# Performance work log

Hardware: AMD Instinct MI355X
Metric: run time of the kernel (lower is better)

The kernel has to match this reference:

```python
import jax, jax.numpy as jnp
import numpy as np

B, N, DIM = 4, 4096, 768
H = 12
DH = DIM // H          # 64
S = 16                 # num_segments
M = N // S             # 256 segment_len
SCALE = DH ** -0.5


def setup_inputs() -> dict:
    key = jax.random.key(0)
    ks = jax.random.split(key, 7)
    std = DIM ** -0.5
    return {
        "x": jax.random.normal(ks[0], (B, N, DIM), dtype=jnp.float32),
        "Wq": jax.random.normal(ks[1], (DIM, DIM), dtype=jnp.float32) * std,
        "Wkv": jax.random.normal(ks[2], (DIM, DIM), dtype=jnp.float32) * std,
        "Wo": jax.random.normal(ks[3], (DIM, DIM), dtype=jnp.float32) * std,
        "bo": jax.random.normal(ks[4], (DIM,), dtype=jnp.float32) * 0.02,
        "Wo0": jax.random.normal(ks[5], (DIM, DIM), dtype=jnp.float32) * std,
        "bo0": jax.random.normal(ks[6], (DIM,), dtype=jnp.float32) * 0.02,
    }


def _rotary_freqs(n, dh, dtype):
    # lucidrains RotaryEmbedding: inv_freq over even dims, emb = cat(freqs, freqs)
    inv_freq = 1.0 / (10000.0 ** (jnp.arange(0, dh, 2, dtype=jnp.float32) / dh))
    t = jnp.arange(n, dtype=jnp.float32)
    freqs = jnp.einsum("n,f->nf", t, inv_freq)           # (n, dh/2)
    return jnp.concatenate([freqs, freqs], axis=-1).astype(dtype)  # (n, dh)


def _rotate_half(t):
    # '... (j d) -> ... j d', j=2 ; (-x2, x1)
    x1, x2 = jnp.split(t, 2, axis=-1)
    return jnp.concatenate([-x2, x1], axis=-1)


def _apply_rotary(freqs, t):
    # freqs: (1, n, dh) broadcast over (bh, n, dh); rot_dim == dh here
    return t * jnp.cos(freqs) + _rotate_half(t) * jnp.sin(freqs)


def reference(x, Wq, Wkv, Wo, bo, Wo0, bo0):
    b, n, dim = x.shape
    q = x @ Wq            # (b, n, dim), bias-free
    kv = x @ Wkv          # shared K==V projection

    def to_heads(t):      # 'b n (h d) -> (b h) n d'
        return t.reshape(b, n, H, DH).transpose(0, 2, 1, 3).reshape(b * H, n, DH)

    q, kv = to_heads(q), to_heads(kv)

    freqs = _rotary_freqs(n, DH, x.dtype)[None, :, :]    # (1, n, dh)
    q = _apply_rotary(freqs, q)
    kv = _apply_rotary(freqs, kv)

    q = q * SCALE
    c = b * H
    qs = q.reshape(c, S, M, DH)
    kvs = kv.reshape(c, S, M, DH)

    # adjacent-segment KV windows: segment t attends to [t-1, t] for t>=1
    kvs_ccs = jnp.concatenate([kvs[:, :-1], kvs[:, 1:]], axis=2)  # (c, S-1, 2M, dh)
    qs_ccs = qs[:, 1:]                                            # (c, S-1, M, dh)

    lsim = jnp.einsum("csmd,csnd->csmn", qs_ccs, kvs_ccs)         # (c, S-1, M, 2M)
    attn1 = jax.nn.softmax(lsim, axis=-1)
    out1 = jnp.einsum("csmn,csnd->csmd", attn1, kvs_ccs)          # (c, S-1, M, dh)

    # global (self) attention within first segment
    q0, kv0 = qs[:, 0], kvs[:, 0]                                 # (c, M, dh)
    sim0 = jnp.einsum("cmd,cnd->cmn", q0, kv0)
    attn0 = jax.nn.softmax(sim0, axis=-1)
    out0 = jnp.einsum("cmn,cnd->cmd", attn0, kv0)                 # (c, M, dh)

    def merge_heads(t, nn):  # '(b h) nn d -> b nn (h d)'
        return t.reshape(b, H, nn, DH).transpose(0, 2, 1, 3).reshape(b, nn, H * DH)

    out_1 = merge_heads(out1.reshape(c, (S - 1) * M, DH), (S - 1) * M)
    out_0 = merge_heads(out0, M)

    out_1o = out_1 @ Wo + bo
    out_0o = out_0 @ Wo0 + bo0
    return jnp.concatenate([out_0o, out_1o], axis=1)              # (b, n, dim)
```

## Files before the change

### kernel.cpp

```cpp
#include <hip/hip_runtime.h>
#include <hip/hip_bf16.h>


typedef float f32x4 __attribute__((ext_vector_type(4)));
typedef short bf16x8 __attribute__((ext_vector_type(8)));

#define DEV static __device__ __forceinline__

DEV short f2bf(float f) {
  union { __hip_bfloat16 h; unsigned short u; } cv;
  cv.h = __float2bfloat16(f);
  return (short)cv.u;
}

DEV f32x4 fz4() { f32x4 z = {0.f, 0.f, 0.f, 0.f}; return z; }

DEV void gload16(const void* g, void* l) {
  __builtin_amdgcn_global_load_lds((const __attribute__((address_space(1))) void*)g,
                                   (__attribute__((address_space(3))) void*)l, 16, 0, 0);
}

__global__ void __launch_bounds__(256) k_rope(float* __restrict__ cosT,
                                              float* __restrict__ sinT) {
  int idx = blockIdx.x * 256 + threadIdx.x;
  int pos = idx >> 5, jm = idx & 31;
  float invf = exp2f(-(float)jm * (13.287712379549449f / 32.0f));
  float th = (float)pos * invf;
  cosT[idx] = cosf(th);
  sinT[idx] = sinf(th);
}

__global__ void __launch_bounds__(256) k_cvtx(const float* __restrict__ x,
                                              short* __restrict__ xb) {
  int i = (blockIdx.x * 256 + threadIdx.x) * 8;
  float4 a = *(const float4*)(x + i);
  float4 b = *(const float4*)(x + i + 4);
  bf16x8 v;
  v[0] = f2bf(a.x); v[1] = f2bf(a.y); v[2] = f2bf(a.z); v[3] = f2bf(a.w);
  v[4] = f2bf(b.x); v[5] = f2bf(b.y); v[6] = f2bf(b.z); v[7] = f2bf(b.w);
  *(bf16x8*)(xb + i) = v;
}

__global__ void __launch_bounds__(256) k_transw(const float* __restrict__ Wq,
                                                const float* __restrict__ Wkv,
                                                const float* __restrict__ Wo,
                                                const float* __restrict__ Wo0,
                                                short* __restrict__ WtQKV,
                                                short* __restrict__ WtO) {
  __shared__ float t[64][65];
  int z = blockIdx.z;
  const float* src = (z == 0) ? Wq : (z == 1) ? Wkv : (z == 2) ? Wo : Wo0;
  short* dst = (z < 2) ? (WtQKV + (size_t)z * (768 * 768))
                       : (WtO + (size_t)(z - 2) * (768 * 768));
  int k0 = blockIdx.x * 64, j0 = blockIdx.y * 64;
  int tc = threadIdx.x & 63, tr = threadIdx.x >> 6;
#pragma unroll
  for (int i = 0; i < 16; i++) {
    int r = i * 4 + tr;
    t[tc][r] = src[(size_t)(k0 + r) * 768 + j0 + tc];
  }
  __syncthreads();
#pragma unroll
  for (int i = 0; i < 16; i++) {
    int r = i * 4 + tr;
    dst[(size_t)(j0 + r) * 768 + k0 + tc] = f2bf(t[r][tc]);
  }
}

#define QSTAGE64(Abuf, Bbuf, Abase, Bbase, kt)                                 \
  {                                                                            \
    int cci = (((tid & 7) ^ ((tid >> 3) & 7)) << 4);                           \
    _Pragma("unroll") for (int i = 0; i < 4; i++) {                            \
      int rowi = i * 32 + (tid >> 3);                                          \
      gload16((Abase) + (size_t)(r0 + rowi) * 1536 + (kt) * 128 + cci,         \
              (char*)(Abuf) + i * 4096 + wid * 1024);                          \
      gload16((Bbase) + (size_t)(j0 + rowi) * 1536 + (kt) * 128 + cci,         \
              (char*)(Bbuf) + i * 4096 + wid * 1024);                          \
    }                                                                          \
  }

__global__ void __launch_bounds__(256, 2) k_gemm_qkv(
    const short* __restrict__ xb, const short* __restrict__ Wt,
    const float* __restrict__ cosT, const float* __restrict__ sinT,
    short* __restrict__ Qb, short* __restrict__ KVb) {
  __shared__ short Al[2][8192];
  __shared__ short Bl[2][8192];
  int bid = blockIdx.x;
  int xcd = bid & 7, loc = bid >> 3;
  int r0 = (xcd * 16 + loc / 12) * 128;
  int cbk = loc % 12;
  bool isQ = cbk < 6;
  int cbl = isQ ? cbk : cbk - 6;
  const char* Ab = (const char*)xb;
  const char* Bb = (const char*)(Wt + (isQ ? (size_t)0 : (size_t)(768 * 768)));
  int j0 = cbl * 128;
  int tid = threadIdx.x, lane = tid & 63, wid = tid >> 6;
  int wr = wid >> 1, wc = wid & 1;
  int l15 = lane & 15, lg = lane >> 4;
  int swz = (l15 & 7) << 4;

  f32x4 acc[4][4];
#pragma unroll
  for (int i = 0; i < 4; i++)
#pragma unroll
    for (int j = 0; j < 4; j++) acc[i][j] = fz4();

  QSTAGE64(Al[0], Bl[0], Ab, Bb, 0)
  for (int kt = 0; kt < 12; kt++) {
    int cb = kt & 1;
    __syncthreads();
    if (kt + 1 < 12) QSTAGE64(Al[cb ^ 1], Bl[cb ^ 1], Ab, Bb, kt + 1)
    const char* Ac = (const char*)Al[cb];
    const char* Bc = (const char*)Bl[cb];
#pragma unroll
    for (int kk = 0; kk < 2; kk++) {
      bf16x8 af[4], bfr[4];
#pragma unroll
      for (int mr = 0; mr < 4; mr++)
        af[mr] = *(const bf16x8*)(Ac + (wr * 64 + mr * 16 + l15) * 128 +
                                  ((kk * 64 + lg * 16) ^ swz));
#pragma unroll
      for (int nc = 0; nc < 4; nc++)
        bfr[nc] = *(const bf16x8*)(Bc + (wc * 64 + nc * 16 + l15) * 128 +
                                   ((kk * 64 + lg * 16) ^ swz));
#pragma unroll
      for (int mr = 0; mr < 4; mr++)
#pragma unroll
        for (int nc = 0; nc < 4; nc++)
          acc[mr][nc] = __builtin_amdgcn_mfma_f32_16x16x32_bf16(af[mr], bfr[nc], acc[mr][nc], 0, 0, 0);
    }
  }

  int h = 2 * cbl + wc;
  short* Ob = isQ ? Qb : KVb;
  float scl = isQ ? 0.18033688011112042f : 1.0f;
#pragma unroll
  for (int mr = 0; mr < 4; mr++) {
#pragma unroll
    for (int rg = 0; rg < 4; rg++) {
      int r = r0 + wr * 64 + mr * 16 + lg * 4 + rg;
      int b = r >> 12, pos = r & 4095;
      const float* cT = cosT + pos * 32;
      const float* sT = sinT + pos * 32;
      float c0 = cT[l15], s0 = sT[l15];
      float c1 = cT[16 + l15], s1 = sT[16 + l15];
      float v0 = acc[mr][0][rg], v1 = acc[mr][1][rg];
      float v2 = acc[mr][2][rg], v3 = acc[mr][3][rg];
      size_t base = ((size_t)((b * 12 + h) * 4096 + pos)) * 64 + l15;
      Ob[base]      = f2bf((v0 * c0 - v2 * s0) * scl);
      Ob[base + 16] = f2bf((v1 * c1 - v3 * s1) * scl);
      Ob[base + 32] = f2bf((v2 * c0 + v0 * s0) * scl);
      Ob[base + 48] = f2bf((v3 * c1 + v1 * s1) * scl);
    }
  }
}

__global__ void __launch_bounds__(256) k_transkv(const short* __restrict__ KVb,
                                                 short* __restrict__ KVt) {
  __shared__ short T[64][72];
  int c = blockIdx.x;
  int pt = blockIdx.y;
  int t = threadIdx.x;
  int ch = t & 7, rr = t >> 3;
#pragma unroll
  for (int i = 0; i < 2; i++) {
    int p = rr + i * 32;
    bf16x8 v = *(const bf16x8*)&KVb[((size_t)c * 4096 + pt * 64 + p) * 64 + ch * 8];
    *(bf16x8*)&T[p][ch * 8] = v;
  }
  __syncthreads();
#pragma unroll
  for (int i = 0; i < 2; i++) {
    int d = rr + i * 32;
    bf16x8 v;
#pragma unroll
    for (int j = 0; j < 8; j++) {
      int cc = ch * 8 + j;
      int g = cc >> 5, sig = cc & 31;
      int p = g * 32 + 4 * (sig >> 3) + (sig & 3) + 16 * ((sig >> 2) & 1);
      v[j] = T[p][d];
    }
    *(bf16x8*)&KVt[((size_t)c * 64 + d) * 4096 + pt * 64 + ch * 8] = v;
  }
}

#define STAGE(buf, kk0)                                                        \
  {                                                                            \
    _Pragma("unroll") for (int i = 0; i < 2; i++) {                            \
      gload16(KVc + (size_t)((kk0) + i * 32 + krow) * 128 + ksrccol,           \
              (char*)Kl[buf] + i * 4096 + wid * 1024);                         \
      gload16(KVtc + ((size_t)(i * 32 + krow) * 4096 + (kk0)) * 2 + ksrccol,   \
              (char*)Vl[buf] + i * 4096 + wid * 1024);                         \
    }                                                                          \
  }

__global__ void __launch_bounds__(256, 4) k_attn(const short* __restrict__ Qb,
                                                 const short* __restrict__ KVbp,
                                                 const short* __restrict__ KVtp,
                                                 short* __restrict__ AO) {
  __shared__ short Kl[2][4096];
  __shared__ short Vl[2][4096];
  int bid = blockIdx.x;
  int orig = (bid & 7) * 192 + (bid >> 3);
  int c = orig >> 5;
  int e = orig & 31;
  int s = (e < 2) ? 0 : ((e - 2) >> 1) + 1;
  int qh = (e < 2) ? e : (e - 2) & 1;
  int NC = (s == 0) ? 4 : 8;
  int Kbase = (s == 0) ? 0 : (s - 1) * 256;

  int tid = threadIdx.x, lane = tid & 63, wid = tid >> 6;
  int l15 = lane & 15, lg = lane >> 4;
  const char* KVc = (const char*)(KVbp + (size_t)c * 4096 * 64);
  const char* KVtc = (const char*)(KVtp + (size_t)c * 64 * 4096);

  int krow = tid >> 3;
  int ksrccol = ((tid & 7) * 16) ^ ((krow & 7) << 4);
  int swz = (l15 & 7) << 4;

  int q0 = s * 256 + qh * 128 + wid * 32;
  bf16x8 qf[2][2];
#pragma unroll
  for (int qt = 0; qt < 2; qt++) {
    const short* Qr = Qb + ((size_t)c * 4096 + q0 + qt * 16 + l15) * 64 + lg * 8;
    qf[qt][0] = *(const bf16x8*)Qr;
    qf[qt][1] = *(const bf16x8*)(Qr + 32);
  }

  const f32x4 mi = {-32.f, -32.f, -32.f, -32.f};
  bf16x8 ones;
#pragma unroll
  for (int j = 0; j < 8; j++) ones[j] = (short)0x3F80;

  f32x4 oacc[2][4];
  f32x4 lacc[2];
#pragma unroll
  for (int qt = 0; qt < 2; qt++) {
    lacc[qt] = fz4();
#pragma unroll
    for (int vt = 0; vt < 4; vt++) oacc[qt][vt] = fz4();
  }

  STAGE(0, Kbase)
  for (int ch = 0; ch < NC; ch++) {
    int cb = ch & 1;
    __syncthreads();
    if (ch + 1 < NC) STAGE(cb ^ 1, Kbase + (ch + 1) * 64)
    const char* Kb_ = (const char*)Kl[cb];
    const char* Vb_ = (const char*)Vl[cb];
#pragma unroll
    for (int u = 0; u < 2; u++) {
      f32x4 z[2][2];
#pragma unroll
      for (int t2 = 0; t2 < 2; t2++) {
        const char* Kp = Kb_ + ((2 * u + t2) * 16 + l15) * 128;
        bf16x8 kf0 = *(const bf16x8*)(Kp + ((lg * 16) ^ swz));
        bf16x8 kf1 = *(const bf16x8*)(Kp + ((64 + lg * 16) ^ swz));
        __builtin_amdgcn_s_setprio(1);
#pragma unroll
        for (int qt = 0; qt < 2; qt++) {
          f32x4 zz = __builtin_amdgcn_mfma_f32_16x16x32_bf16(kf0, qf[qt][0], mi, 0, 0, 0);
          zz = __builtin_amdgcn_mfma_f32_16x16x32_bf16(kf1, qf[qt][1], zz, 0, 0, 0);
          z[qt][t2] = zz;
        }
        __builtin_amdgcn_s_setprio(0);
      }
      bf16x8 pf[2];
#pragma unroll
      for (int qt = 0; qt < 2; qt++) {
#pragma unroll
        for (int t2 = 0; t2 < 2; t2++)
#pragma unroll
          for (int r = 0; r < 4; r++)
            pf[qt][t2 * 4 + r] = f2bf(exp2f(z[qt][t2][r]));
      }
      bf16x8 vf[4];
#pragma unroll
      for (int vt = 0; vt < 4; vt++)
        vf[vt] = *(const bf16x8*)(Vb_ + (vt * 16 + l15) * 128 +
                                  ((u * 64 + lg * 16) ^ swz));
      __builtin_amdgcn_s_setprio(1);
#pragma unroll
      for (int qt = 0; qt < 2; qt++) {
#pragma unroll
        for (int vt = 0; vt < 4; vt++)
          oacc[qt][vt] = __builtin_amdgcn_mfma_f32_16x16x32_bf16(pf[qt], vf[vt], oacc[qt][vt], 0, 0, 0);
        lacc[qt] = __builtin_amdgcn_mfma_f32_16x16x32_bf16(pf[qt], ones, lacc[qt], 0, 0, 0);
      }
      __builtin_amdgcn_s_setprio(0);
    }
  }

  int bq = c / 12, hh = c % 12;
#pragma unroll
  for (int qt = 0; qt < 2; qt++) {
    float rinv[4];
#pragma unroll
    for (int r = 0; r < 4; r++) rinv[r] = 1.0f / lacc[qt][r];
#pragma unroll
    for (int vt = 0; vt < 4; vt++)
#pragma unroll
      for (int r = 0; r < 4; r++) {
        size_t row = (size_t)bq * 4096 + q0 + qt * 16 + lg * 4 + r;
        AO[row * 768 + hh * 64 + vt * 16 + l15] = f2bf(oacc[qt][vt][r] * rinv[r]);
      }
  }
}

__global__ void __launch_bounds__(256, 2) k_gemm_out(
    const short* __restrict__ AO, const short* __restrict__ Wt,
    const float* __restrict__ bo, const float* __restrict__ bo0,
    float* __restrict__ out) {
  __shared__ short Al[2][8192];
  __shared__ short Bl[2][8192];
  int bid = blockIdx.x;
  int xcd = bid & 7, loc = bid >> 3;
  int r0 = (xcd * 16 + loc / 6) * 128;
  int j0 = (loc % 6) * 128;
  bool o0sel = (r0 & 4095) < 256;
  const char* Ab = (const char*)AO;
  const char* Bb = (const char*)(Wt + (o0sel ? (size_t)1 : (size_t)0) * (768 * 768));
  const float* bias = o0sel ? bo0 : bo;
  int tid = threadIdx.x, lane = tid & 63, wid = tid >> 6;
  int wr = wid >> 1, wc = wid & 1;
  int l15 = lane & 15, lg = lane >> 4;
  int swz = (l15 & 7) << 4;

  f32x4 acc[4][4];
#pragma unroll
  for (int i = 0; i < 4; i++)
#pragma unroll
    for (int j = 0; j < 4; j++) acc[i][j] = fz4();

  QSTAGE64(Al[0], Bl[0], Ab, Bb, 0)
  for (int kt = 0; kt < 12; kt++) {
    int cb = kt & 1;
    __syncthreads();
    if (kt + 1 < 12) QSTAGE64(Al[cb ^ 1], Bl[cb ^ 1], Ab, Bb, kt + 1)
    const char* Ac = (const char*)Al[cb];
    const char* Bc = (const char*)Bl[cb];
#pragma unroll
    for (int kk = 0; kk < 2; kk++) {
      bf16x8 af[4], bfr[4];
#pragma unroll
      for (int mr = 0; mr < 4; mr++)
        af[mr] = *(const bf16x8*)(Ac + (wr * 64 + mr * 16 + l15) * 128 +
                                  ((kk * 64 + lg * 16) ^ swz));
#pragma unroll
      for (int nc = 0; nc < 4; nc++)
        bfr[nc] = *(const bf16x8*)(Bc + (wc * 64 + nc * 16 + l15) * 128 +
                                   ((kk * 64 + lg * 16) ^ swz));
#pragma unroll
      for (int mr = 0; mr < 4; mr++)
#pragma unroll
        for (int nc = 0; nc < 4; nc++)
          acc[mr][nc] = __builtin_amdgcn_mfma_f32_16x16x32_bf16(af[mr], bfr[nc], acc[mr][nc], 0, 0, 0);
    }
  }

  float bs[4];
#pragma unroll
  for (int nc = 0; nc < 4; nc++) bs[nc] = bias[j0 + wc * 64 + nc * 16 + l15];
#pragma unroll
  for (int mr = 0; mr < 4; mr++)
#pragma unroll
    for (int rg = 0; rg < 4; rg++) {
      size_t r = (size_t)r0 + wr * 64 + mr * 16 + lg * 4 + rg;
      float* op = out + r * 768 + j0 + wc * 64 + l15;
      op[0]  = acc[mr][0][rg] + bs[0];
      op[16] = acc[mr][1][rg] + bs[1];
      op[32] = acc[mr][2][rg] + bs[2];
      op[48] = acc[mr][3][rg] + bs[3];
    }
}

extern "C" void kernel_launch(void* const* d_in, const int* in_sizes, int n_in,
                              void* d_out, int out_size, void* d_ws, size_t ws_size,
                              hipStream_t stream) {
  (void)in_sizes; (void)n_in; (void)out_size; (void)ws_size;
  const float* x   = (const float*)d_in[0];
  const float* Wq  = (const float*)d_in[1];
  const float* Wkv = (const float*)d_in[2];
  const float* Wo  = (const float*)d_in[3];
  const float* bo  = (const float*)d_in[4];
  const float* Wo0 = (const float*)d_in[5];
  const float* bo0 = (const float*)d_in[6];
  float* out = (float*)d_out;

  char* ws = (char*)d_ws;
  short* xb    = (short*)(ws + 0);
  short* AO    = xb;
  short* Qb    = (short*)(ws + 25165824);
  short* KVb   = (short*)(ws + 50331648);
  short* KVt   = (short*)(ws + 75497472);
  short* WtQKV = (short*)(ws + 75497472);
  float* cosT  = (float*)(ws + 77856768);
  float* sinT  = (float*)(ws + 78381056);
  short* WtO   = (short*)(ws + 100663296);

  k_rope<<<512, 256, 0, stream>>>(cosT, sinT);
  k_cvtx<<<6144, 256, 0, stream>>>(x, xb);
  k_transw<<<dim3(12, 12, 4), 256, 0, stream>>>(Wq, Wkv, Wo, Wo0, WtQKV, WtO);
  k_gemm_qkv<<<1536, 256, 0, stream>>>(xb, WtQKV, cosT, sinT, Qb, KVb);
  k_transkv<<<dim3(48, 64), 256, 0, stream>>>(KVb, KVt);
  k_attn<<<1536, 256, 0, stream>>>(Qb, KVb, KVt, AO);
  k_gemm_out<<<768, 256, 0, stream>>>(AO, WtO, bo, bo0, out);
}
```

Baseline: 160.0 us.

## Fuse KV transpose into QKV GEMM epilogue and interleave rope cos/sin tables

The QKV GEMM epilogue now also writes the transposed KV layout itself, staging tiles through shared memory with a permuted, swizzled order, so the separate k_transkv kernel launch and its extra read of KVb are dropped. The rope cos and sin tables are merged into one float2 array so each epilogue lookup is a single load. Workspace offsets are rearranged and the fused path is used only when the workspace is large enough. Otherwise it falls back to the old separate transpose. The cost is an extra LDS round trip and two barriers in the KV blocks' epilogue.

```diff
diff --git a/kernel.cpp b/kernel.cpp
--- a/kernel.cpp
+++ b/kernel.cpp
@@ -20,14 +20,12 @@
                                    (__attribute__((address_space(3))) void*)l, 16, 0, 0);
 }
 
-__global__ void __launch_bounds__(256) k_rope(float* __restrict__ cosT,
-                                              float* __restrict__ sinT) {
+__global__ void __launch_bounds__(256) k_rope(float2* __restrict__ csT) {
   int idx = blockIdx.x * 256 + threadIdx.x;
   int pos = idx >> 5, jm = idx & 31;
   float invf = exp2f(-(float)jm * (13.287712379549449f / 32.0f));
   float th = (float)pos * invf;
-  cosT[idx] = cosf(th);
-  sinT[idx] = sinf(th);
+  csT[idx] = make_float2(cosf(th), sinf(th));
 }
 
 __global__ void __launch_bounds__(256) k_cvtx(const float* __restrict__ x,
@@ -81,10 +79,10 @@
 
 __global__ void __launch_bounds__(256, 2) k_gemm_qkv(
     const short* __restrict__ xb, const short* __restrict__ Wt,
-    const float* __restrict__ cosT, const float* __restrict__ sinT,
-    short* __restrict__ Qb, short* __restrict__ KVb) {
-  __shared__ short Al[2][8192];
-  __shared__ short Bl[2][8192];
+    const float2* __restrict__ csT,
+    short* __restrict__ Qb, short* __restrict__ KVb,
+    short* __restrict__ KVtw) {
+  __shared__ short Lsh[4][8192];
   int bid = blockIdx.x;
   int xcd = bid & 7, loc = bid >> 3;
   int r0 = (xcd * 16 + loc / 12) * 128;
@@ -105,13 +103,13 @@
 #pragma unroll
     for (int j = 0; j < 4; j++) acc[i][j] = fz4();
 
-  QSTAGE64(Al[0], Bl[0], Ab, Bb, 0)
+  QSTAGE64(Lsh[0], Lsh[2], Ab, Bb, 0)
   for (int kt = 0; kt < 12; kt++) {
     int cb = kt & 1;
     __syncthreads();
-    if (kt + 1 < 12) QSTAGE64(Al[cb ^ 1], Bl[cb ^ 1], Ab, Bb, kt + 1)
-    const char* Ac = (const char*)Al[cb];
-    const char* Bc = (const char*)Bl[cb];
+    if (kt + 1 < 12) QSTAGE64(Lsh[cb ^ 1], Lsh[2 + (cb ^ 1)], Ab, Bb, kt + 1)
+    const char* Ac = (const char*)Lsh[cb];
+    const char* Bc = (const char*)Lsh[2 + cb];
 #pragma unroll
     for (int kk = 0; kk < 2; kk++) {
       bf16x8 af[4], bfr[4];
@@ -134,23 +132,56 @@
   int h = 2 * cbl + wc;
   short* Ob = isQ ? Qb : KVb;
   float scl = isQ ? 0.18033688011112042f : 1.0f;
+  short ovv[4][4][4];
 #pragma unroll
   for (int mr = 0; mr < 4; mr++) {
 #pragma unroll
     for (int rg = 0; rg < 4; rg++) {
       int r = r0 + wr * 64 + mr * 16 + lg * 4 + rg;
       int b = r >> 12, pos = r & 4095;
-      const float* cT = cosT + pos * 32;
-      const float* sT = sinT + pos * 32;
-      float c0 = cT[l15], s0 = sT[l15];
-      float c1 = cT[16 + l15], s1 = sT[16 + l15];
+      const float2* cp = csT + pos * 32;
+      float2 cs0 = cp[l15], cs1 = cp[16 + l15];
       float v0 = acc[mr][0][rg], v1 = acc[mr][1][rg];
       float v2 = acc[mr][2][rg], v3 = acc[mr][3][rg];
+      short o0 = f2bf((v0 * cs0.x - v2 * cs0.y) * scl);
+      short o1 = f2bf((v1 * cs1.x - v3 * cs1.y) * scl);
+      short o2 = f2bf((v2 * cs0.x + v0 * cs0.y) * scl);
+      short o3 = f2bf((v3 * cs1.x + v1 * cs1.y) * scl);
       size_t base = ((size_t)((b * 12 + h) * 4096 + pos)) * 64 + l15;
-      Ob[base]      = f2bf((v0 * c0 - v2 * s0) * scl);
-      Ob[base + 16] = f2bf((v1 * c1 - v3 * s1) * scl);
-      Ob[base + 32] = f2bf((v2 * c0 + v0 * s0) * scl);
-      Ob[base + 48] = f2bf((v3 * c1 + v1 * s1) * scl);
+      Ob[base] = o0; Ob[base + 16] = o1; Ob[base + 32] = o2; Ob[base + 48] = o3;
+      ovv[mr][rg][0] = o0; ovv[mr][rg][1] = o1;
+      ovv[mr][rg][2] = o2; ovv[mr][rg][3] = o3;
+    }
+  }
+
+  if (!isQ && KVtw) {
+    __syncthreads();
+    short* Ovt = (short*)Lsh;
+#pragma unroll
+    for (int mr = 0; mr < 4; mr++)
+#pragma unroll
+      for (int rg = 0; rg < 4; rg++) {
+        int p = wr * 64 + mr * 16 + lg * 4 + rg;
+        int w = p & 31, g = p >> 5;
+        int sig = 8 * ((w & 15) >> 2) + 4 * ((w >> 4) & 1) + (w & 3);
+        int pi = g * 32 + sig;
+#pragma unroll
+        for (int nc = 0; nc < 4; nc++) {
+          int row = wc * 64 + nc * 16 + l15;
+          Ovt[row * 136 + (pi ^ ((row & 3) << 4))] = ovv[mr][rg][nc];
+        }
+      }
+    __syncthreads();
+    int b = r0 >> 12, pos0 = r0 & 4095;
+#pragma unroll
+    for (int z = 0; z < 8; z++) {
+      int rr = z * 16 + (tid >> 4);
+      int chunk = tid & 15;
+      int off = rr * 136 + ((chunk * 8) ^ ((rr & 3) << 4));
+      bf16x8 v = *(const bf16x8*)&Ovt[off];
+      int wcr = rr >> 6, d = rr & 63;
+      *(bf16x8*)&KVtw[((size_t)((b * 12 + 2 * cbl + wcr) * 64 + d)) * 4096 +
+                      pos0 + chunk * 8] = v;
     }
   }
 }
@@ -311,8 +342,7 @@
     const short* __restrict__ AO, const short* __restrict__ Wt,
     const float* __restrict__ bo, const float* __restrict__ bo0,
     float* __restrict__ out) {
-  __shared__ short Al[2][8192];
-  __shared__ short Bl[2][8192];
+  __shared__ short Lsh[4][8192];
   int bid = blockIdx.x;
   int xcd = bid & 7, loc = bid >> 3;
   int r0 = (xcd * 16 + loc / 6) * 128;
@@ -332,13 +362,13 @@
 #pragma unroll
     for (int j = 0; j < 4; j++) acc[i][j] = fz4();
 
-  QSTAGE64(Al[0], Bl[0], Ab, Bb, 0)
+  QSTAGE64(Lsh[0], Lsh[2], Ab, Bb, 0)
   for (int kt = 0; kt < 12; kt++) {
     int cb = kt & 1;
     __syncthreads();
-    if (kt + 1 < 12) QSTAGE64(Al[cb ^ 1], Bl[cb ^ 1], Ab, Bb, kt + 1)
-    const char* Ac = (const char*)Al[cb];
-    const char* Bc = (const char*)Bl[cb];
+    if (kt + 1 < 12) QSTAGE64(Lsh[cb ^ 1], Lsh[2 + (cb ^ 1)], Ab, Bb, kt + 1)
+    const char* Ac = (const char*)Lsh[cb];
+    const char* Bc = (const char*)Lsh[2 + cb];
 #pragma unroll
     for (int kk = 0; kk < 2; kk++) {
       bf16x8 af[4], bfr[4];
@@ -377,7 +407,7 @@
 extern "C" void kernel_launch(void* const* d_in, const int* in_sizes, int n_in,
                               void* d_out, int out_size, void* d_ws, size_t ws_size,
                               hipStream_t stream) {
-  (void)in_sizes; (void)n_in; (void)out_size; (void)ws_size;
+  (void)in_sizes; (void)n_in; (void)out_size;
   const float* x   = (const float*)d_in[0];
   const float* Wq  = (const float*)d_in[1];
   const float* Wkv = (const float*)d_in[2];
@@ -388,21 +418,31 @@
   float* out = (float*)d_out;
 
   char* ws = (char*)d_ws;
-  short* xb    = (short*)(ws + 0);
-  short* AO    = xb;
-  short* Qb    = (short*)(ws + 25165824);
-  short* KVb   = (short*)(ws + 50331648);
-  short* KVt   = (short*)(ws + 75497472);
-  short* WtQKV = (short*)(ws + 75497472);
-  float* cosT  = (float*)(ws + 77856768);
-  float* sinT  = (float*)(ws + 78381056);
-  short* WtO   = (short*)(ws + 100663296);
-
-  k_rope<<<512, 256, 0, stream>>>(cosT, sinT);
+  short* xb  = (short*)(ws + 0);
+  short* AO  = xb;
+  short* Qb  = (short*)(ws + 25165824);
+  short* KVb = (short*)(ws + 50331648);
+  short* KVt = (short*)(ws + 75497472);
+
+  bool fused = ws_size >= 106430464u;
+  float2* csT;
+  short *WtQKV, *WtO;
+  if (fused) {
+    csT   = (float2*)(ws + 100663296);
+    WtQKV = (short*)(ws + 101711872);
+    WtO   = (short*)(ws + 104071168);
+  } else {
+    WtQKV = (short*)(ws + 75497472);
+    csT   = (float2*)(ws + 77856768);
+    WtO   = (short*)(ws + 100663296);
+  }
+
+  k_rope<<<512, 256, 0, stream>>>(csT);
   k_cvtx<<<6144, 256, 0, stream>>>(x, xb);
   k_transw<<<dim3(12, 12, 4), 256, 0, stream>>>(Wq, Wkv, Wo, Wo0, WtQKV, WtO);
-  k_gemm_qkv<<<1536, 256, 0, stream>>>(xb, WtQKV, cosT, sinT, Qb, KVb);
-  k_transkv<<<dim3(48, 64), 256, 0, stream>>>(KVb, KVt);
+  k_gemm_qkv<<<1536, 256, 0, stream>>>(xb, WtQKV, csT, Qb, KVb,
+                                       fused ? KVt : (short*)nullptr);
+  if (!fused) k_transkv<<<dim3(48, 64), 256, 0, stream>>>(KVb, KVt);
   k_attn<<<1536, 256, 0, stream>>>(Qb, KVb, KVt, AO);
   k_gemm_out<<<768, 256, 0, stream>>>(AO, WtO, bo, bo0, out);
 }
```

Measured after the change: 150.4 us. -6.0%, faster.
